# Kernel optimization log

Hardware: AMD Instinct MI355X
Metric: run time of the kernel (lower is better)

The kernel has to match this reference:

```python
import jax, jax.numpy as jnp
import numpy as np

SEQ, B, XD = 2048, 4, 16
D, NH, DFF, L, M = 256, 8, 512, 2, 1024
DH = D // NH
NEG_INF = -1e9  # finite stand-in for -inf (same softmax result, grad-safe)


def setup_inputs() -> dict:
    key = jax.random.key(0)
    ks = iter(jax.random.split(key, 40))

    def w(shape, s=0.02):
        return jax.random.normal(next(ks), shape, dtype=jnp.float32) * s

    return {
        "x": jax.random.normal(next(ks), (SEQ, B, XD), dtype=jnp.float32),
        "y": jax.random.normal(next(ks), (SEQ, B), dtype=jnp.float32),
        "single_eval_pos": M,
        "xenc_w": w((D, XD)), "xenc_b": w((D,)),
        "yenc_w": w((D, 1)), "yenc_b": w((D,)),
        "in_proj_w": w((L, 3 * D, D)), "in_proj_b": w((L, 3 * D)),
        "out_proj_w": w((L, D, D)), "out_proj_b": w((L, D)),
        "ln1_g": jnp.ones((L, D), jnp.float32), "ln1_b": jnp.zeros((L, D), jnp.float32),
        "lin1_w": w((L, DFF, D)), "lin1_b": w((L, DFF)),
        "lin2_w": w((L, D, DFF)), "lin2_b": w((L, D)),
        "ln2_g": jnp.ones((L, D), jnp.float32), "ln2_b": jnp.zeros((L, D), jnp.float32),
        "head_w1": w((DFF, D)), "head_b1": w((DFF,)),
        "head_w2": w((1, DFF)), "head_b2": w((1,)),
    }


def _layer_norm(x, g, b, eps=1e-5):
    mu = jnp.mean(x, axis=-1, keepdims=True)
    var = jnp.var(x, axis=-1, keepdims=True)
    return (x - mu) * jax.lax.rsqrt(var + eps) * g + b


def _forward(x, y, M_, p):
    seq, batch = y.shape
    x_src = x @ p["xenc_w"].T + p["xenc_b"]                     # [seq, b, D]
    y_src = y[..., None] @ p["yenc_w"].T + p["yenc_b"]           # [seq, b, D]
    tokens = jnp.concatenate([x_src[:M_] + y_src[:M_], x_src[M_:]], axis=0)

    # prefix-block + diagonal mask: keep (j < M) or (i == j)
    i = jnp.arange(seq)
    keep = (i[None, :] < M_) | (i[:, None] == i[None, :])
    mask = jnp.where(keep, 0.0, NEG_INF).astype(tokens.dtype)    # [seq, seq]

    h = tokens
    for l in range(p["in_proj_w"].shape[0]):
        qkv = h @ p["in_proj_w"][l].T + p["in_proj_b"][l]        # [seq, b, 3D]
        q, k, v = jnp.split(qkv, 3, axis=-1)
        to_heads = lambda t: t.reshape(seq, batch, NH, DH).transpose(1, 2, 0, 3)
        q, k, v = to_heads(q), to_heads(k), to_heads(v)          # [b, h, s, dh]
        scores = jnp.einsum("bhqd,bhkd->bhqk", q, k) / np.float32(np.sqrt(DH)) + mask
        attn = jax.nn.softmax(scores, axis=-1)
        o = jnp.einsum("bhqk,bhkd->bhqd", attn, v)
        o = o.transpose(2, 0, 1, 3).reshape(seq, batch, D)
        o = o @ p["out_proj_w"][l].T + p["out_proj_b"][l]
        h = _layer_norm(h + o, p["ln1_g"][l], p["ln1_b"][l])      # post-norm
        ff = jax.nn.gelu(h @ p["lin1_w"][l].T + p["lin1_b"][l], approximate=False)
        ff = ff @ p["lin2_w"][l].T + p["lin2_b"][l]
        h = _layer_norm(h + ff, p["ln2_g"][l], p["ln2_b"][l])

    q_out = h[M_:]                                               # [seq-M, b, D]
    hid = jax.nn.gelu(q_out @ p["head_w1"].T + p["head_b1"], approximate=False)
    return hid @ p["head_w2"].T + p["head_b2"]                   # [seq-M, b, 1]


def reference(x, y, single_eval_pos, xenc_w, xenc_b, yenc_w, yenc_b,
              in_proj_w, in_proj_b, out_proj_w, out_proj_b,
              ln1_g, ln1_b, lin1_w, lin1_b, lin2_w, lin2_b, ln2_g, ln2_b,
              head_w1, head_b1, head_w2, head_b2):
    p = dict(xenc_w=xenc_w, xenc_b=xenc_b, yenc_w=yenc_w, yenc_b=yenc_b,
             in_proj_w=in_proj_w, in_proj_b=in_proj_b,
             out_proj_w=out_proj_w, out_proj_b=out_proj_b,
             ln1_g=ln1_g, ln1_b=ln1_b, lin1_w=lin1_w, lin1_b=lin1_b,
             lin2_w=lin2_w, lin2_b=lin2_b, ln2_g=ln2_g, ln2_b=ln2_b,
             head_w1=head_w1, head_b1=head_b1, head_w2=head_w2, head_b2=head_b2)
    return _forward(x, y, int(single_eval_pos), p)
```

## Files before the change

kernel.cpp:

```cpp
#include <hip/hip_runtime.h>
#include <hip/hip_bf16.h>
#include <math.h>

#define SEQ    2048
#define BATCH  4
#define XDIM   16
#define DMODEL 256
#define NHEAD  8
#define DH     32
#define DFF    512
#define NLAYER 2
#define MPOS   1024
#define ROWS   (SEQ*BATCH)

#define ATT_SCALE 0.17677669529663687f
#define BK 32

typedef __attribute__((ext_vector_type(8))) short bf16x8;
typedef __attribute__((ext_vector_type(4))) float f32x4;

__device__ __forceinline__ float gelu_exact(float x) {
    return 0.5f * x * (1.0f + erff(x * 0.70710678118654752f));
}
__device__ __forceinline__ short f2bf(float f) {
    unsigned int u = __float_as_uint(f);
    u += 0x7FFFu + ((u >> 16) & 1u);
    return (short)(u >> 16);
}
__device__ __forceinline__ float bf2f(unsigned short u) {
    return __uint_as_float(((unsigned int)u) << 16);
}
__device__ __forceinline__ void gload16(const unsigned short* g, unsigned short* l) {
    __builtin_amdgcn_global_load_lds(
        (const __attribute__((address_space(1))) unsigned int*)g,
        (__attribute__((address_space(3))) unsigned int*)l, 16, 0, 0);
}
#define VMWAIT(N) asm volatile("s_waitcnt vmcnt(" #N ")" ::: "memory")
__device__ __forceinline__ void pipe_barrier() {
    __builtin_amdgcn_sched_barrier(0);
    __builtin_amdgcn_s_barrier();
    __builtin_amdgcn_sched_barrier(0);
}

__global__ __launch_bounds__(256) void encode_cast(
    const float* __restrict__ x, const float* __restrict__ y,
    const float* __restrict__ xw, const float* __restrict__ xb,
    const float* __restrict__ yw, const float* __restrict__ yb,
    float* __restrict__ h, unsigned short* __restrict__ hb,
    const float* __restrict__ s0, const float* __restrict__ s1,
    const float* __restrict__ s2, const float* __restrict__ s3,
    const float* __restrict__ s4,
    unsigned short* __restrict__ d0, unsigned short* __restrict__ d1,
    unsigned short* __restrict__ d2, unsigned short* __restrict__ d3,
    unsigned short* __restrict__ d4)
{
    if (blockIdx.x < ROWS/4) {
        int g = blockIdx.x;
        int d = threadIdx.x;
        __shared__ float xs[4][XDIM];
        __shared__ float ys[4];
        if (d < 64) xs[d>>4][d&15] = x[(size_t)(g*4 + (d>>4))*XDIM + (d&15)];
        if (d < 4)  ys[d] = y[g*4 + d];
        __syncthreads();
        float wreg[XDIM];
        #pragma unroll
        for (int k = 0; k < XDIM; ++k) wreg[k] = xw[d*XDIM + k];
        const float xbv = xb[d], ywv = yw[d], ybv = yb[d];
        const bool train = (g < MPOS);
        #pragma unroll
        for (int r = 0; r < 4; ++r) {
            int row = g*4 + r;
            float acc = xbv;
            #pragma unroll
            for (int k = 0; k < XDIM; ++k) acc = fmaf(xs[r][k], wreg[k], acc);
            if (train) acc += ys[r]*ywv + ybv;
            h[(size_t)row*DMODEL + d]  = acc;
            hb[(size_t)row*DMODEL + d] = (unsigned short)f2bf(acc);
        }
        return;
    }
    int i = (blockIdx.x - ROWS/4)*256 + threadIdx.x;
    if (i >= 147456) return;
    const float* s; unsigned short* d; int off;
    if      (i <  49152) { s = s0; d = d0; off = i; }
    else if (i <  65536) { s = s1; d = d1; off = i - 49152; }
    else if (i <  98304) { s = s2; d = d2; off = i - 65536; }
    else if (i < 131072) { s = s3; d = d3; off = i - 98304; }
    else                 { s = s4; d = d4; off = i - 131072; }
    float4 a = *(const float4*)(s + (size_t)off*8);
    float4 c = *(const float4*)(s + (size_t)off*8 + 4);
    ushort4 u0, u1;
    u0.x=(unsigned short)f2bf(a.x); u0.y=(unsigned short)f2bf(a.y);
    u0.z=(unsigned short)f2bf(a.z); u0.w=(unsigned short)f2bf(a.w);
    u1.x=(unsigned short)f2bf(c.x); u1.y=(unsigned short)f2bf(c.y);
    u1.z=(unsigned short)f2bf(c.z); u1.w=(unsigned short)f2bf(c.w);
    *(ushort4*)(d + (size_t)off*8)     = u0;
    *(ushort4*)(d + (size_t)off*8 + 4) = u1;
}

__global__ __launch_bounds__(256) void gemm_qkv(
    const unsigned short* __restrict__ A, const unsigned short* __restrict__ B,
    const float* __restrict__ bias,
    unsigned short* __restrict__ Qg, unsigned short* __restrict__ Kg,
    unsigned short* __restrict__ Vg, int K)
{
    __shared__ unsigned short As[3][128][BK];
    __shared__ unsigned short Bs[3][64][BK];
    int tid  = threadIdx.x;
    int w    = tid >> 6, lane = tid & 63;
    int col  = lane & 15, quad = lane >> 4;
    int u    = blockIdx.x >> 3, xcd = blockIdx.x & 7;
    int by   = xcd*8 + u/12, bx = u%12;
    int m0   = by * 128, n0 = bx * 64;
    int l4   = lane >> 2, c8 = (lane & 3) * 8;

    f32x4 acc[2][4];
    #pragma unroll
    for (int i = 0; i < 2; ++i)
        #pragma unroll
        for (int j = 0; j < 4; ++j) acc[i][j] = (f32x4){0.f,0.f,0.f,0.f};

    const unsigned short* ga = A + (size_t)(m0 + w*32 + l4)*K + c8;
    const unsigned short* gb = B + (size_t)(n0 + w*16 + l4)*K + c8;

    const int NS = K / BK;
    gload16(ga,                  &As[0][w*32     ][0]);
    gload16(ga + (size_t)16*K,   &As[0][w*32 + 16][0]);
    gload16(gb,                  &Bs[0][w*16     ][0]);
    gload16(ga + BK,                  &As[1][w*32     ][0]);
    gload16(ga + BK + (size_t)16*K,   &As[1][w*32 + 16][0]);
    gload16(gb + BK,                  &Bs[1][w*16     ][0]);

    int bcur = 0;
    for (int s = 0; s < NS; ++s) {
        if (s == NS - 1) { VMWAIT(0); } else { VMWAIT(3); }
        pipe_barrier();
        if (s + 2 < NS) {
            int bpre = bcur + 2; if (bpre >= 3) bpre -= 3;
            int k2 = (s + 2) * BK;
            gload16(ga + k2,                &As[bpre][w*32     ][0]);
            gload16(ga + k2 + (size_t)16*K, &As[bpre][w*32 + 16][0]);
            gload16(gb + k2,                &Bs[bpre][w*16     ][0]);
        }
        bf16x8 af[2], bfr[4];
        #pragma unroll
        for (int i = 0; i < 2; ++i) af[i]  = *(const bf16x8*)&As[bcur][w*32 + i*16 + col][quad*8];
        #pragma unroll
        for (int j = 0; j < 4; ++j) bfr[j] = *(const bf16x8*)&Bs[bcur][j*16 + col][quad*8];
        #pragma unroll
        for (int i = 0; i < 2; ++i)
            #pragma unroll
            for (int j = 0; j < 4; ++j)
                acc[i][j] = __builtin_amdgcn_mfma_f32_16x16x32_bf16(bfr[j], af[i], acc[i][j], 0, 0, 0);
        bcur = (bcur == 2) ? 0 : bcur + 1;
    }

    int region = n0 >> 8;
    if (region < 2) {
        #pragma unroll
        for (int i = 0; i < 2; ++i) {
            int m = m0 + w*32 + i*16 + col;
            int s = m >> 2, bidx = m & 3;
            #pragma unroll
            for (int j = 0; j < 4; ++j) {
                int ng = n0 + j*16 + quad*4;
                float4 bi = *(const float4*)&bias[ng];
                ushort4 uu;
                uu.x=(unsigned short)f2bf(acc[i][j][0] + bi.x);
                uu.y=(unsigned short)f2bf(acc[i][j][1] + bi.y);
                uu.z=(unsigned short)f2bf(acc[i][j][2] + bi.z);
                uu.w=(unsigned short)f2bf(acc[i][j][3] + bi.w);
                int np = ng - (region << 8);
                int hh = np >> 5, d = np & 31;
                int bh = bidx*NHEAD + hh;
                if (region == 0)
                    *(ushort4*)(Qg + ((size_t)(bh*SEQ + s))*DH + d) = uu;
                else
                    *(ushort4*)(Kg + ((size_t)(bh*SEQ + s))*DH + d) = uu;
            }
        }
    } else {
        __syncthreads();
        unsigned short* T3 = (unsigned short*)As;
        #pragma unroll
        for (int i = 0; i < 2; ++i) {
            int mi = w*32 + i*16 + col;
            int ss = mi >> 2, bidx = mi & 3;
            #pragma unroll
            for (int j = 0; j < 4; ++j) {
                int ni = j*16 + quad*4;
                float4 bi = *(const float4*)&bias[n0 + ni];
                T3[((ni    )*4 + bidx)*32 + ss] = (unsigned short)f2bf(acc[i][j][0] + bi.x);
                T3[((ni + 1)*4 + bidx)*32 + ss] = (unsigned short)f2bf(acc[i][j][1] + bi.y);
                T3[((ni + 2)*4 + bidx)*32 + ss] = (unsigned short)f2bf(acc[i][j][2] + bi.z);
                T3[((ni + 3)*4 + bidx)*32 + ss] = (unsigned short)f2bf(acc[i][j][3] + bi.w);
            }
        }
        __syncthreads();
        int sBase = m0 >> 2;
        #pragma unroll
        for (int r = 0; r < 4; ++r) {
            int chunk = tid + 256*r;
            int l = chunk >> 2, p = chunk & 3;
            int d = l & 31, hh_l = (l >> 5) & 1, bidx = l >> 6;
            int ni = hh_l*32 + d;
            int hh = ((n0 & 255) + ni) >> 5;
            int bh = bidx*NHEAD + hh;
            uint4 val = *(const uint4*)&T3[(ni*4 + bidx)*32 + p*8];
            *(uint4*)(Vg + ((size_t)(bh*DH + d))*SEQ + sBase + p*8) = val;
        }
    }
}

__global__ __launch_bounds__(256) void attn_mfma(
    const unsigned short* __restrict__ Qg,
    const unsigned short* __restrict__ Kg,
    const unsigned short* __restrict__ Vg,
    unsigned short* __restrict__ o)
{
    const int id  = blockIdx.x;
    const int sl  = id >> 3;
    const int bh  = (id & 7) * 4 + (sl >> 4);
    const int qt2 = sl & 15;
    const int h   = bh & 7;
    const int b   = bh >> 3;
    const int q0A = qt2 * 64;
    const int q0B = MPOS + qt2 * 64;
    const int tid  = threadIdx.x;
    const int w    = tid >> 6;
    const int lane = tid & 63;
    const int col  = lane & 15;
    const int quad = lane >> 4;

    __shared__ unsigned short Kt[2][64][40];
    __shared__ unsigned short Vt[2][32][72];
    __shared__ unsigned short PtA[4][16][72];
    __shared__ unsigned short PtB[4][16][72];

    const int qA = q0A + 16*w + col;
    const int qB = q0B + 16*w + col;
    bf16x8 qfA = *(const bf16x8*)(Qg + ((size_t)(bh*SEQ + qA))*DH + quad*8);
    bf16x8 qfB = *(const bf16x8*)(Qg + ((size_t)(bh*SEQ + qB))*DH + quad*8);

    f32x4 O0A = {0.f,0.f,0.f,0.f}, O1A = {0.f,0.f,0.f,0.f};
    f32x4 O0B = {0.f,0.f,0.f,0.f}, O1B = {0.f,0.f,0.f,0.f};
    float lsumA = 0.f, lsumB = 0.f;

    const int kRow = tid >> 2, kCh = (tid & 3) * 8;
    const int vD   = tid >> 3, vCh = (tid & 7) * 8;

    uint4 kreg = *(const uint4*)(Kg + ((size_t)(bh*SEQ + kRow))*DH + kCh);
    uint4 vreg = *(const uint4*)(Vg + ((size_t)(bh*DH + vD))*SEQ + vCh);

    for (int kt = 0; kt < 17; ++kt) {
        const bool self = (kt == 16);
        const int  p    = kt & 1;
        *(uint4*)&Kt[p][kRow][kCh] = kreg;
        *(uint4*)&Vt[p][vD][vCh]   = vreg;
        __syncthreads();
        if (kt < 16) {
            int kn = (kt == 15) ? q0B : (kt + 1)*64;
            kreg = *(const uint4*)(Kg + ((size_t)(bh*SEQ + kn + kRow))*DH + kCh);
            vreg = *(const uint4*)(Vg + ((size_t)(bh*DH + vD))*SEQ + kn + vCh);
        }

        #pragma unroll
        for (int mt = 0; mt < 4; ++mt) {
            bf16x8 kf = *(const bf16x8*)&Kt[p][mt*16 + col][quad*8];
            if (!self) {
                f32x4 stA = {0.f,0.f,0.f,0.f};
                stA = __builtin_amdgcn_mfma_f32_16x16x32_bf16(kf, qfA, stA, 0, 0, 0);
                ushort4 pwA;
                #pragma unroll
                for (int i = 0; i < 4; ++i) {
                    float pv = __expf(stA[i]*ATT_SCALE);
                    unsigned short us = (unsigned short)f2bf(pv);
                    ((unsigned short*)&pwA)[i] = us;
                    lsumA += bf2f(us);
                }
                *(ushort4*)&PtA[w][col][mt*16 + quad*4] = pwA;
            }
            f32x4 stB = {0.f,0.f,0.f,0.f};
            stB = __builtin_amdgcn_mfma_f32_16x16x32_bf16(kf, qfB, stB, 0, 0, 0);
            ushort4 pwB;
            #pragma unroll
            for (int i = 0; i < 4; ++i) {
                float pv = __expf(stB[i]*ATT_SCALE);
                if (self && (mt*16 + quad*4 + i != 16*w + col)) pv = 0.f;
                unsigned short us = (unsigned short)f2bf(pv);
                ((unsigned short*)&pwB)[i] = us;
                lsumB += bf2f(us);
            }
            *(ushort4*)&PtB[w][col][mt*16 + quad*4] = pwB;
        }
        #pragma unroll
        for (int c = 0; c < 2; ++c) {
            bf16x8 v0 = *(const bf16x8*)&Vt[p][col     ][c*32 + quad*8];
            bf16x8 v1 = *(const bf16x8*)&Vt[p][col + 16][c*32 + quad*8];
            if (!self) {
                bf16x8 pfA = *(const bf16x8*)&PtA[w][col][c*32 + quad*8];
                O0A = __builtin_amdgcn_mfma_f32_16x16x32_bf16(v0, pfA, O0A, 0, 0, 0);
                O1A = __builtin_amdgcn_mfma_f32_16x16x32_bf16(v1, pfA, O1A, 0, 0, 0);
            }
            bf16x8 pfB = *(const bf16x8*)&PtB[w][col][c*32 + quad*8];
            O0B = __builtin_amdgcn_mfma_f32_16x16x32_bf16(v0, pfB, O0B, 0, 0, 0);
            O1B = __builtin_amdgcn_mfma_f32_16x16x32_bf16(v1, pfB, O1B, 0, 0, 0);
        }
    }

    lsumA += __shfl_xor(lsumA, 16, 64); lsumA += __shfl_xor(lsumA, 32, 64);
    lsumB += __shfl_xor(lsumB, 16, 64); lsumB += __shfl_xor(lsumB, 32, 64);
    float invA = 1.0f / lsumA, invB = 1.0f / lsumB;
    ushort4 u0, u1;
    #pragma unroll
    for (int i = 0; i < 4; ++i) {
        ((unsigned short*)&u0)[i] = (unsigned short)f2bf(O0A[i]*invA);
        ((unsigned short*)&u1)[i] = (unsigned short)f2bf(O1A[i]*invA);
    }
    unsigned short* opA = o + ((size_t)(qA*BATCH + b))*DMODEL + h*DH;
    *(ushort4*)(opA + quad*4)      = u0;
    *(ushort4*)(opA + 16 + quad*4) = u1;
    #pragma unroll
    for (int i = 0; i < 4; ++i) {
        ((unsigned short*)&u0)[i] = (unsigned short)f2bf(O0B[i]*invB);
        ((unsigned short*)&u1)[i] = (unsigned short)f2bf(O1B[i]*invB);
    }
    unsigned short* opB = o + ((size_t)(qB*BATCH + b))*DMODEL + h*DH;
    *(ushort4*)(opB + quad*4)      = u0;
    *(ushort4*)(opB + 16 + quad*4) = u1;
}

__global__ __launch_bounds__(256) void mlp_fused(
    const unsigned short* __restrict__ attb,
    const unsigned short* __restrict__ Wout, const float* __restrict__ ob,
    const float* __restrict__ g1, const float* __restrict__ be1,
    const unsigned short* __restrict__ W1, const float* __restrict__ fb1,
    const unsigned short* __restrict__ W2, const float* __restrict__ fb2,
    const float* __restrict__ g2, const float* __restrict__ be2,
    float* __restrict__ h, unsigned short* __restrict__ hb,
    const unsigned short* __restrict__ Wh1, const float* __restrict__ hb1,
    const float* __restrict__ hw2, const float* __restrict__ hb2,
    float* __restrict__ out, int doHead)
{
    __shared__ unsigned short Bs[3][256][BK];
    __shared__ unsigned short As[3][2][16][BK];
    __shared__ unsigned short Ht[2][16][264];
    __shared__ unsigned short Pt[2][16][520];
    __shared__ float sP[2][4][16], qP[2][4][16];

    const int tid  = threadIdx.x;
    const int w    = tid >> 6;
    const int lane = tid & 63;
    const int col  = lane & 15;
    const int quad = lane >> 4;
    const int l4   = lane >> 2;
    const int c8   = (lane & 3) * 8;
    const int bid  = blockIdx.x;
    const int m0a  = bid * 16;
    const int m0b  = 4096 + bid * 16;
    const int ma   = m0a + col;
    const int mb   = m0b + col;

    float resid[2][4][4];

    {
        f32x4 acc[2][4];
        #pragma unroll
        for (int g = 0; g < 2; ++g)
            #pragma unroll
            for (int j = 0; j < 4; ++j) acc[g][j] = (f32x4){0.f,0.f,0.f,0.f};

        const unsigned short* ga0 = attb + (size_t)(m0a + l4)*DMODEL + c8;
        const unsigned short* ga1 = attb + (size_t)(m0b + l4)*DMODEL + c8;
        const unsigned short* gb  = Wout + (size_t)(w*64 + l4)*DMODEL + c8;
        const int NS = DMODEL / BK;

        #pragma unroll
        for (int pb = 0; pb < 2; ++pb) {
            int k = pb * BK;
            if (w == 0) {
                gload16(ga0 + k, &As[pb][0][0][0]);
                gload16(ga1 + k, &As[pb][1][0][0]);
            }
            #pragma unroll
            for (int rr = 0; rr < 4; ++rr)
                gload16(gb + k + (size_t)(rr*16)*DMODEL, &Bs[pb][w*64 + rr*16][0]);
        }
        int bcur = 0;
        for (int s = 0; s < NS; ++s) {
            if (s == NS - 1)  { VMWAIT(0); }
            else if (w == 0)  { VMWAIT(6); }
            else              { VMWAIT(4); }
            pipe_barrier();
            if (s + 2 < NS) {
                int bpre = bcur + 2; if (bpre >= 3) bpre -= 3;
                int k2 = (s + 2) * BK;
                if (w == 0) {
                    gload16(ga0 + k2, &As[bpre][0][0][0]);
                    gload16(ga1 + k2, &As[bpre][1][0][0]);
                }
                #pragma unroll
                for (int rr = 0; rr < 4; ++rr)
                    gload16(gb + k2 + (size_t)(rr*16)*DMODEL, &Bs[bpre][w*64 + rr*16][0]);
            }
            bf16x8 af0 = *(const bf16x8*)&As[bcur][0][col][quad*8];
            bf16x8 af1 = *(const bf16x8*)&As[bcur][1][col][quad*8];
            #pragma unroll
            for (int j = 0; j < 4; ++j) {
                bf16x8 bfr = *(const bf16x8*)&Bs[bcur][w*64 + j*16 + col][quad*8];
                acc[0][j] = __builtin_amdgcn_mfma_f32_16x16x32_bf16(bfr, af0, acc[0][j], 0, 0, 0);
                acc[1][j] = __builtin_amdgcn_mfma_f32_16x16x32_bf16(bfr, af1, acc[1][j], 0, 0, 0);
            }
            bcur = (bcur == 2) ? 0 : bcur + 1;
        }

        float ssum[2] = {0.f, 0.f}, qsum[2] = {0.f, 0.f};
        #pragma unroll
        for (int g = 0; g < 2; ++g) {
            int m = g ? mb : ma;
            #pragma unroll
            for (int j = 0; j < 4; ++j) {
                int n = w*64 + j*16 + quad*4;
                float4 bi = *(const float4*)&ob[n];
                float4 hv = *(const float4*)&h[(size_t)m*DMODEL + n];
                #pragma unroll
                for (int i = 0; i < 4; ++i) {
                    float val = acc[g][j][i] + ((const float*)&bi)[i] + ((const float*)&hv)[i];
                    resid[g][j][i] = val;
                    ssum[g] += val; qsum[g] += val*val;
                }
            }
        }
        #pragma unroll
        for (int g = 0; g < 2; ++g) {
            ssum[g] += __shfl_xor(ssum[g], 16, 64); ssum[g] += __shfl_xor(ssum[g], 32, 64);
            qsum[g] += __shfl_xor(qsum[g], 16, 64); qsum[g] += __shfl_xor(qsum[g], 32, 64);
        }
        if (quad == 0) {
            sP[0][w][col] = ssum[0]; qP[0][w][col] = qsum[0];
            sP[1][w][col] = ssum[1]; qP[1][w][col] = qsum[1];
        }
        __syncthreads();
        #pragma unroll
        for (int g = 0; g < 2; ++g) {
            float st = sP[g][0][col] + sP[g][1][col] + sP[g][2][col] + sP[g][3][col];
            float qt = qP[g][0][col] + qP[g][1][col] + qP[g][2][col] + qP[g][3][col];
            float mu   = st * (1.0f/DMODEL);
            float var  = qt * (1.0f/DMODEL) - mu*mu;
            float rstd = rsqrtf(var + 1e-5f);
            #pragma unroll
            for (int j = 0; j < 4; ++j) {
                int n = w*64 + j*16 + quad*4;
                float4 gv = *(const float4*)&g1[n];
                float4 bv = *(const float4*)&be1[n];
                ushort4 u;
                #pragma unroll
                for (int i = 0; i < 4; ++i) {
                    float o = (resid[g][j][i]-mu)*rstd*((const float*)&gv)[i] + ((const float*)&bv)[i];
                    resid[g][j][i] = o;
                    ((unsigned short*)&u)[i] = (unsigned short)f2bf(o);
                }
                *(ushort4*)&Ht[g][col][n] = u;
            }
        }
        __syncthreads();
    }

    #pragma unroll 1
    for (int nh = 0; nh < 2; ++nh) {
        f32x4 acc[2][4];
        #pragma unroll
        for (int g = 0; g < 2; ++g)
            #pragma unroll
            for (int j = 0; j < 4; ++j) acc[g][j] = (f32x4){0.f,0.f,0.f,0.f};
        const unsigned short* gb = W1 + (size_t)(nh*256 + w*64 + l4)*DMODEL + c8;
        const int NS = DMODEL / BK;

        #pragma unroll
        for (int pb = 0; pb < 2; ++pb)
            #pragma unroll
            for (int rr = 0; rr < 4; ++rr)
                gload16(gb + pb*BK + (size_t)(rr*16)*DMODEL, &Bs[pb][w*64 + rr*16][0]);

        int bcur = 0;
        for (int s = 0; s < NS; ++s) {
            if (s == NS - 1) { VMWAIT(0); } else { VMWAIT(4); }
            pipe_barrier();
            if (s + 2 < NS) {
                int bpre = bcur + 2; if (bpre >= 3) bpre -= 3;
                int k2 = (s + 2) * BK;
                #pragma unroll
                for (int rr = 0; rr < 4; ++rr)
                    gload16(gb + k2 + (size_t)(rr*16)*DMODEL, &Bs[bpre][w*64 + rr*16][0]);
            }
            bf16x8 af0 = *(const bf16x8*)&Ht[0][col][s*BK + quad*8];
            bf16x8 af1 = *(const bf16x8*)&Ht[1][col][s*BK + quad*8];
            #pragma unroll
            for (int j = 0; j < 4; ++j) {
                bf16x8 bfr = *(const bf16x8*)&Bs[bcur][w*64 + j*16 + col][quad*8];
                acc[0][j] = __builtin_amdgcn_mfma_f32_16x16x32_bf16(bfr, af0, acc[0][j], 0, 0, 0);
                acc[1][j] = __builtin_amdgcn_mfma_f32_16x16x32_bf16(bfr, af1, acc[1][j], 0, 0, 0);
            }
            bcur = (bcur == 2) ? 0 : bcur + 1;
        }
        #pragma unroll
        for (int g = 0; g < 2; ++g)
            #pragma unroll
            for (int j = 0; j < 4; ++j) {
                int n2 = nh*256 + w*64 + j*16 + quad*4;
                float4 bi = *(const float4*)&fb1[n2];
                ushort4 u;
                #pragma unroll
                for (int i = 0; i < 4; ++i)
                    ((unsigned short*)&u)[i] = (unsigned short)f2bf(gelu_exact(acc[g][j][i] + ((const float*)&bi)[i]));
                *(ushort4*)&Pt[g][col][n2] = u;
            }
        pipe_barrier();
    }

    {
        __syncthreads();
        f32x4 acc[2][4];
        #pragma unroll
        for (int g = 0; g < 2; ++g)
            #pragma unroll
            for (int j = 0; j < 4; ++j) acc[g][j] = (f32x4){0.f,0.f,0.f,0.f};
        const unsigned short* gb = W2 + (size_t)(w*64 + l4)*DFF + c8;
        const int NS = DFF / BK;

        #pragma unroll
        for (int pb = 0; pb < 2; ++pb)
            #pragma unroll
            for (int rr = 0; rr < 4; ++rr)
                gload16(gb + pb*BK + (size_t)(rr*16)*DFF, &Bs[pb][w*64 + rr*16][0]);

        int bcur = 0;
        for (int s = 0; s < NS; ++s) {
            if (s == NS - 1) { VMWAIT(0); } else { VMWAIT(4); }
            pipe_barrier();
            if (s + 2 < NS) {
                int bpre = bcur + 2; if (bpre >= 3) bpre -= 3;
                int k2 = (s + 2) * BK;
                #pragma unroll
                for (int rr = 0; rr < 4; ++rr)
                    gload16(gb + k2 + (size_t)(rr*16)*DFF, &Bs[bpre][w*64 + rr*16][0]);
            }
            bf16x8 af0 = *(const bf16x8*)&Pt[0][col][s*BK + quad*8];
            bf16x8 af1 = *(const bf16x8*)&Pt[1][col][s*BK + quad*8];
            #pragma unroll
            for (int j = 0; j < 4; ++j) {
                bf16x8 bfr = *(const bf16x8*)&Bs[bcur][w*64 + j*16 + col][quad*8];
                acc[0][j] = __builtin_amdgcn_mfma_f32_16x16x32_bf16(bfr, af0, acc[0][j], 0, 0, 0);
                acc[1][j] = __builtin_amdgcn_mfma_f32_16x16x32_bf16(bfr, af1, acc[1][j], 0, 0, 0);
            }
            bcur = (bcur == 2) ? 0 : bcur + 1;
        }

        float ssum[2] = {0.f, 0.f}, qsum[2] = {0.f, 0.f};
        #pragma unroll
        for (int g = 0; g < 2; ++g)
            #pragma unroll
            for (int j = 0; j < 4; ++j) {
                int n = w*64 + j*16 + quad*4;
                float4 bi = *(const float4*)&fb2[n];
                #pragma unroll
                for (int i = 0; i < 4; ++i) {
                    float val = acc[g][j][i] + ((const float*)&bi)[i] + resid[g][j][i];
                    resid[g][j][i] = val;
                    ssum[g] += val; qsum[g] += val*val;
                }
            }
        #pragma unroll
        for (int g = 0; g < 2; ++g) {
            ssum[g] += __shfl_xor(ssum[g], 16, 64); ssum[g] += __shfl_xor(ssum[g], 32, 64);
            qsum[g] += __shfl_xor(qsum[g], 16, 64); qsum[g] += __shfl_xor(qsum[g], 32, 64);
        }
        if (quad == 0) {
            sP[0][w][col] = ssum[0]; qP[0][w][col] = qsum[0];
            sP[1][w][col] = ssum[1]; qP[1][w][col] = qsum[1];
        }
        __syncthreads();
        #pragma unroll
        for (int g = 0; g < 2; ++g) {
            int m = g ? mb : ma;
            float st = sP[g][0][col] + sP[g][1][col] + sP[g][2][col] + sP[g][3][col];
            float qt = qP[g][0][col] + qP[g][1][col] + qP[g][2][col] + qP[g][3][col];
            float mu   = st * (1.0f/DMODEL);
            float var  = qt * (1.0f/DMODEL) - mu*mu;
            float rstd = rsqrtf(var + 1e-5f);
            #pragma unroll
            for (int j = 0; j < 4; ++j) {
                int n = w*64 + j*16 + quad*4;
                float4 gv = *(const float4*)&g2[n];
                float4 bv = *(const float4*)&be2[n];
                float4 o;
                ushort4 u;
                #pragma unroll
                for (int i = 0; i < 4; ++i) {
                    float ov = (resid[g][j][i]-mu)*rstd*((const float*)&gv)[i] + ((const float*)&bv)[i];
                    ((float*)&o)[i] = ov;
                    ((unsigned short*)&u)[i] = (unsigned short)f2bf(ov);
                }
                *(float4*)&h[(size_t)m*DMODEL + n] = o;
                *(ushort4*)(hb + (size_t)m*DMODEL + n) = u;
                *(ushort4*)&Ht[g][col][n] = u;
            }
        }
        __syncthreads();
    }

    if (doHead) {
        float sdot = 0.f;
        #pragma unroll 1
        for (int nh = 0; nh < 2; ++nh) {
            f32x4 acc[4];
            #pragma unroll
            for (int j = 0; j < 4; ++j) acc[j] = (f32x4){0.f,0.f,0.f,0.f};
            const unsigned short* gb = Wh1 + (size_t)(nh*256 + w*64 + l4)*DMODEL + c8;
            const int NS = DMODEL / BK;

            #pragma unroll
            for (int pb = 0; pb < 2; ++pb)
                #pragma unroll
                for (int rr = 0; rr < 4; ++rr)
                    gload16(gb + pb*BK + (size_t)(rr*16)*DMODEL, &Bs[pb][w*64 + rr*16][0]);

            int bcur = 0;
            for (int s = 0; s < NS; ++s) {
                if (s == NS - 1) { VMWAIT(0); } else { VMWAIT(4); }
                pipe_barrier();
                if (s + 2 < NS) {
                    int bpre = bcur + 2; if (bpre >= 3) bpre -= 3;
                    int k2 = (s + 2) * BK;
                    #pragma unroll
                    for (int rr = 0; rr < 4; ++rr)
                        gload16(gb + k2 + (size_t)(rr*16)*DMODEL, &Bs[bpre][w*64 + rr*16][0]);
                }
                bf16x8 af = *(const bf16x8*)&Ht[1][col][s*BK + quad*8];
                #pragma unroll
                for (int j = 0; j < 4; ++j) {
                    bf16x8 bfr = *(const bf16x8*)&Bs[bcur][w*64 + j*16 + col][quad*8];
                    acc[j] = __builtin_amdgcn_mfma_f32_16x16x32_bf16(bfr, af, acc[j], 0, 0, 0);
                }
                bcur = (bcur == 2) ? 0 : bcur + 1;
            }
            #pragma unroll
            for (int j = 0; j < 4; ++j) {
                int n2 = nh*256 + w*64 + j*16 + quad*4;
                float4 b1v = *(const float4*)&hb1[n2];
                float4 w2v = *(const float4*)&hw2[n2];
                #pragma unroll
                for (int i = 0; i < 4; ++i)
                    sdot += gelu_exact(acc[j][i] + ((const float*)&b1v)[i]) * ((const float*)&w2v)[i];
            }
            pipe_barrier();
        }
        sdot += __shfl_xor(sdot, 16, 64); sdot += __shfl_xor(sdot, 32, 64);
        if (quad == 0) sP[0][w][col] = sdot;
        __syncthreads();
        if (tid < 16)
            out[bid*16 + tid] = sP[0][0][tid] + sP[0][1][tid] + sP[0][2][tid] + sP[0][3][tid] + hb2[0];
    }
}

extern "C" void kernel_launch(void* const* d_in, const int* in_sizes, int n_in,
                              void* d_out, int out_size, void* d_ws, size_t ws_size,
                              hipStream_t stream)
{
    const float* x        = (const float*)d_in[0];
    const float* y        = (const float*)d_in[1];
    const float* xenc_w   = (const float*)d_in[3];
    const float* xenc_b   = (const float*)d_in[4];
    const float* yenc_w   = (const float*)d_in[5];
    const float* yenc_b   = (const float*)d_in[6];
    const float* in_proj_w  = (const float*)d_in[7];
    const float* in_proj_b  = (const float*)d_in[8];
    const float* out_proj_w = (const float*)d_in[9];
    const float* out_proj_b = (const float*)d_in[10];
    const float* ln1_g    = (const float*)d_in[11];
    const float* ln1_b    = (const float*)d_in[12];
    const float* lin1_w   = (const float*)d_in[13];
    const float* lin1_b   = (const float*)d_in[14];
    const float* lin2_w   = (const float*)d_in[15];
    const float* lin2_b   = (const float*)d_in[16];
    const float* ln2_g    = (const float*)d_in[17];
    const float* ln2_b    = (const float*)d_in[18];
    const float* head_w1  = (const float*)d_in[19];
    const float* head_b1  = (const float*)d_in[20];
    const float* head_w2  = (const float*)d_in[21];
    const float* head_b2  = (const float*)d_in[22];
    float* out = (float*)d_out;

    float* ws  = (float*)d_ws;
    float* h    = ws;
    unsigned short* hb    = (unsigned short*)(h + (size_t)ROWS*DMODEL);
    unsigned short* attb  = hb    + (size_t)ROWS*DMODEL;
    unsigned short* Qg    = attb  + (size_t)ROWS*DMODEL;
    unsigned short* Kg    = Qg    + (size_t)BATCH*NHEAD*SEQ*DH;
    unsigned short* Vg    = Kg    + (size_t)BATCH*NHEAD*SEQ*DH;
    unsigned short* Wqkv  = Vg    + (size_t)BATCH*NHEAD*SEQ*DH;
    unsigned short* Wout  = Wqkv  + (size_t)NLAYER*3*DMODEL*DMODEL;
    unsigned short* Wl1   = Wout  + (size_t)NLAYER*DMODEL*DMODEL;
    unsigned short* Wl2   = Wl1   + (size_t)NLAYER*DFF*DMODEL;
    unsigned short* Wh1   = Wl2   + (size_t)NLAYER*DMODEL*DFF;

    encode_cast<<<ROWS/4 + 576, 256, 0, stream>>>(
        x, y, xenc_w, xenc_b, yenc_w, yenc_b, h, hb,
        in_proj_w, out_proj_w, lin1_w, lin2_w, head_w1,
        Wqkv, Wout, Wl1, Wl2, Wh1);

    for (int l = 0; l < NLAYER; ++l) {
        gemm_qkv<<<768, 256, 0, stream>>>(
            hb, Wqkv + (size_t)l*3*DMODEL*DMODEL, in_proj_b + l*3*DMODEL,
            Qg, Kg, Vg, DMODEL);
        attn_mfma<<<512, 256, 0, stream>>>(Qg, Kg, Vg, attb);
        mlp_fused<<<256, 256, 0, stream>>>(
            attb,
            Wout + (size_t)l*DMODEL*DMODEL, out_proj_b + l*DMODEL,
            ln1_g + l*DMODEL, ln1_b + l*DMODEL,
            Wl1 + (size_t)l*DFF*DMODEL, lin1_b + l*DFF,
            Wl2 + (size_t)l*DMODEL*DFF, lin2_b + l*DMODEL,
            ln2_g + l*DMODEL, ln2_b + l*DMODEL,
            h, hb,
            Wh1, head_b1, head_w2, head_b2,
            out, (l == NLAYER-1) ? 1 : 0);
    }
}
```

Before: 258.9 us.

## Fuse layer-1 QKV projection into layer-0 MLP kernel epilogue

For the first layer, the fused MLP kernel now also computes the next layer's QKV projection. It reuses the normalized hidden tile still held in shared memory (Ht) and writes Q, K and V directly in head layout, which removes one gemm_qkv launch and its reread of hb. The cost is more work per block on only 256 blocks instead of 768. The V writes are scalar transposed stores, which may be poorly coalesced.

```diff
diff --git a/kernel.cpp b/kernel.cpp
--- a/kernel.cpp
+++ b/kernel.cpp
@@ -340,7 +340,10 @@
     float* __restrict__ h, unsigned short* __restrict__ hb,
     const unsigned short* __restrict__ Wh1, const float* __restrict__ hb1,
     const float* __restrict__ hw2, const float* __restrict__ hb2,
-    float* __restrict__ out, int doHead)
+    float* __restrict__ out, int doHead,
+    const unsigned short* __restrict__ Wq, const float* __restrict__ qbias,
+    unsigned short* __restrict__ Qg, unsigned short* __restrict__ Kg,
+    unsigned short* __restrict__ Vg, int doQkv)
 {
     __shared__ unsigned short Bs[3][256][BK];
     __shared__ unsigned short As[3][2][16][BK];
@@ -660,6 +663,76 @@
         __syncthreads();
         if (tid < 16)
             out[bid*16 + tid] = sP[0][0][tid] + sP[0][1][tid] + sP[0][2][tid] + sP[0][3][tid] + hb2[0];
+    }
+
+    if (doQkv) {
+        #pragma unroll 1
+        for (int r = 0; r < 3; ++r) {
+            f32x4 acc[2][4];
+            #pragma unroll
+            for (int g = 0; g < 2; ++g)
+                #pragma unroll
+                for (int j = 0; j < 4; ++j) acc[g][j] = (f32x4){0.f,0.f,0.f,0.f};
+            const unsigned short* gb = Wq + (size_t)(r*256 + w*64 + l4)*DMODEL + c8;
+            const int NS = DMODEL / BK;
+
+            #pragma unroll
+            for (int pb = 0; pb < 2; ++pb)
+                #pragma unroll
+                for (int rr = 0; rr < 4; ++rr)
+                    gload16(gb + pb*BK + (size_t)(rr*16)*DMODEL, &Bs[pb][w*64 + rr*16][0]);
+
+            int bcur = 0;
+            for (int s = 0; s < NS; ++s) {
+                if (s == NS - 1) { VMWAIT(0); } else { VMWAIT(4); }
+                pipe_barrier();
+                if (s + 2 < NS) {
+                    int bpre = bcur + 2; if (bpre >= 3) bpre -= 3;
+                    int k2 = (s + 2) * BK;
+                    #pragma unroll
+                    for (int rr = 0; rr < 4; ++rr)
+                        gload16(gb + k2 + (size_t)(rr*16)*DMODEL, &Bs[bpre][w*64 + rr*16][0]);
+                }
+                bf16x8 af0 = *(const bf16x8*)&Ht[0][col][s*BK + quad*8];
+                bf16x8 af1 = *(const bf16x8*)&Ht[1][col][s*BK + quad*8];
+                #pragma unroll
+                for (int j = 0; j < 4; ++j) {
+                    bf16x8 bfr = *(const bf16x8*)&Bs[bcur][w*64 + j*16 + col][quad*8];
+                    acc[0][j] = __builtin_amdgcn_mfma_f32_16x16x32_bf16(bfr, af0, acc[0][j], 0, 0, 0);
+                    acc[1][j] = __builtin_amdgcn_mfma_f32_16x16x32_bf16(bfr, af1, acc[1][j], 0, 0, 0);
+                }
+                bcur = (bcur == 2) ? 0 : bcur + 1;
+            }
+
+            #pragma unroll
+            for (int g = 0; g < 2; ++g) {
+                int m = (g ? m0b : m0a) + col;
+                int ss = m >> 2, bidx = m & 3;
+                #pragma unroll
+                for (int j = 0; j < 4; ++j) {
+                    int n32 = w*64 + j*16 + quad*4;
+                    float4 bi = *(const float4*)&qbias[r*256 + n32];
+                    ushort4 u;
+                    u.x = (unsigned short)f2bf(acc[g][j][0] + bi.x);
+                    u.y = (unsigned short)f2bf(acc[g][j][1] + bi.y);
+                    u.z = (unsigned short)f2bf(acc[g][j][2] + bi.z);
+                    u.w = (unsigned short)f2bf(acc[g][j][3] + bi.w);
+                    int hh = n32 >> 5, d = n32 & 31;
+                    int bh = bidx*NHEAD + hh;
+                    if (r == 0)
+                        *(ushort4*)(Qg + ((size_t)(bh*SEQ + ss))*DH + d) = u;
+                    else if (r == 1)
+                        *(ushort4*)(Kg + ((size_t)(bh*SEQ + ss))*DH + d) = u;
+                    else {
+                        Vg[((size_t)(bh*DH + d    ))*SEQ + ss] = u.x;
+                        Vg[((size_t)(bh*DH + d + 1))*SEQ + ss] = u.y;
+                        Vg[((size_t)(bh*DH + d + 2))*SEQ + ss] = u.z;
+                        Vg[((size_t)(bh*DH + d + 3))*SEQ + ss] = u.w;
+                    }
+                }
+            }
+            pipe_barrier();
+        }
     }
 }
 
@@ -710,9 +783,9 @@
         Wqkv, Wout, Wl1, Wl2, Wh1);
 
     for (int l = 0; l < NLAYER; ++l) {
-        gemm_qkv<<<768, 256, 0, stream>>>(
-            hb, Wqkv + (size_t)l*3*DMODEL*DMODEL, in_proj_b + l*3*DMODEL,
-            Qg, Kg, Vg, DMODEL);
+        if (l == 0)
+            gemm_qkv<<<768, 256, 0, stream>>>(
+                hb, Wqkv, in_proj_b, Qg, Kg, Vg, DMODEL);
         attn_mfma<<<512, 256, 0, stream>>>(Qg, Kg, Vg, attb);
         mlp_fused<<<256, 256, 0, stream>>>(
             attb,
@@ -723,6 +796,8 @@
             ln2_g + l*DMODEL, ln2_b + l*DMODEL,
             h, hb,
             Wh1, head_b1, head_w2, head_b2,
-            out, (l == NLAYER-1) ? 1 : 0);
-    }
-}
+            out, (l == NLAYER-1) ? 1 : 0,
+            Wqkv + (size_t)3*DMODEL*DMODEL, in_proj_b + 3*DMODEL,
+            Qg, Kg, Vg, (l == 0) ? 1 : 0);
+    }
+}
```

New measurement: 265.8 us. +2.7%, slower.

## Widen mlp_fused K-tile to 64 with XOR-swizzled LDS and aliased A/P buffers

Applied to the files above, without the earlier changes.

Doubles the K step of every GEMM stage in the fused MLP kernel from 32 to 64, which halves the number of pipeline barriers and waits per GEMM. Weight and activation tiles are stored in LDS with an XOR swizzle on 16-byte chunks so that MFMA fragment reads avoid bank conflicts. All four waves now share the activation-tile loads, where before only wave 0 issued them. The As staging buffer and the Pt GELU buffer share one aliased LDS region to offset the larger Bs. The cost is more LDS per block and more loads in flight per stage, which could reduce occupancy.

```diff
diff --git a/kernel.cpp b/kernel.cpp
--- a/kernel.cpp
+++ b/kernel.cpp
@@ -342,19 +342,23 @@
     const float* __restrict__ hw2, const float* __restrict__ hb2,
     float* __restrict__ out, int doHead)
 {
-    __shared__ unsigned short Bs[3][256][BK];
-    __shared__ unsigned short As[3][2][16][BK];
+    __shared__ unsigned short Bs[3][256][64];
+    __shared__ __align__(16) unsigned char smem_u[33280];
     __shared__ unsigned short Ht[2][16][264];
-    __shared__ unsigned short Pt[2][16][520];
     __shared__ float sP[2][4][16], qP[2][4][16];
+
+    typedef unsigned short AsT[2][16][64];
+    AsT* As = reinterpret_cast<AsT*>(smem_u);
+    typedef unsigned short PtT[16][520];
+    PtT* Pt = reinterpret_cast<PtT*>(smem_u);
 
     const int tid  = threadIdx.x;
     const int w    = tid >> 6;
     const int lane = tid & 63;
     const int col  = lane & 15;
     const int quad = lane >> 4;
-    const int l4   = lane >> 2;
-    const int c8   = (lane & 3) * 8;
+    const int l8   = lane >> 3;
+    const int c8s  = (((lane & 7) ^ l8) * 8);
     const int bid  = blockIdx.x;
     const int m0a  = bid * 16;
     const int m0b  = 4096 + bid * 16;
@@ -370,46 +374,42 @@
             #pragma unroll
             for (int j = 0; j < 4; ++j) acc[g][j] = (f32x4){0.f,0.f,0.f,0.f};
 
-        const unsigned short* ga0 = attb + (size_t)(m0a + l4)*DMODEL + c8;
-        const unsigned short* ga1 = attb + (size_t)(m0b + l4)*DMODEL + c8;
-        const unsigned short* gb  = Wout + (size_t)(w*64 + l4)*DMODEL + c8;
-        const int NS = DMODEL / BK;
+        const int gr = w >> 1;
+        const unsigned short* gaw = attb + (size_t)((gr ? m0b : m0a) + (w&1)*8 + l8)*DMODEL + c8s;
+        const unsigned short* gb  = Wout + (size_t)(w*64 + l8)*DMODEL + c8s;
+        const int NS = DMODEL / 64;
 
         #pragma unroll
         for (int pb = 0; pb < 2; ++pb) {
-            int k = pb * BK;
-            if (w == 0) {
-                gload16(ga0 + k, &As[pb][0][0][0]);
-                gload16(ga1 + k, &As[pb][1][0][0]);
-            }
-            #pragma unroll
-            for (int rr = 0; rr < 4; ++rr)
-                gload16(gb + k + (size_t)(rr*16)*DMODEL, &Bs[pb][w*64 + rr*16][0]);
+            int k = pb * 64;
+            gload16(gaw + k, &As[pb][gr][(w&1)*8][0]);
+            #pragma unroll
+            for (int t = 0; t < 8; ++t)
+                gload16(gb + k + (size_t)(t*8)*DMODEL, &Bs[pb][w*64 + t*8][0]);
         }
         int bcur = 0;
         for (int s = 0; s < NS; ++s) {
-            if (s == NS - 1)  { VMWAIT(0); }
-            else if (w == 0)  { VMWAIT(6); }
-            else              { VMWAIT(4); }
+            if (s == NS - 1) { VMWAIT(0); } else { VMWAIT(9); }
             pipe_barrier();
             if (s + 2 < NS) {
                 int bpre = bcur + 2; if (bpre >= 3) bpre -= 3;
-                int k2 = (s + 2) * BK;
-                if (w == 0) {
-                    gload16(ga0 + k2, &As[bpre][0][0][0]);
-                    gload16(ga1 + k2, &As[bpre][1][0][0]);
-                }
-                #pragma unroll
-                for (int rr = 0; rr < 4; ++rr)
-                    gload16(gb + k2 + (size_t)(rr*16)*DMODEL, &Bs[bpre][w*64 + rr*16][0]);
-            }
-            bf16x8 af0 = *(const bf16x8*)&As[bcur][0][col][quad*8];
-            bf16x8 af1 = *(const bf16x8*)&As[bcur][1][col][quad*8];
-            #pragma unroll
-            for (int j = 0; j < 4; ++j) {
-                bf16x8 bfr = *(const bf16x8*)&Bs[bcur][w*64 + j*16 + col][quad*8];
-                acc[0][j] = __builtin_amdgcn_mfma_f32_16x16x32_bf16(bfr, af0, acc[0][j], 0, 0, 0);
-                acc[1][j] = __builtin_amdgcn_mfma_f32_16x16x32_bf16(bfr, af1, acc[1][j], 0, 0, 0);
+                int k2 = (s + 2) * 64;
+                gload16(gaw + k2, &As[bpre][gr][(w&1)*8][0]);
+                #pragma unroll
+                for (int t = 0; t < 8; ++t)
+                    gload16(gb + k2 + (size_t)(t*8)*DMODEL, &Bs[bpre][w*64 + t*8][0]);
+            }
+            #pragma unroll
+            for (int kk = 0; kk < 2; ++kk) {
+                const int so = (((kk*4 + quad) ^ (col & 7)) * 8);
+                bf16x8 af0 = *(const bf16x8*)&As[bcur][0][col][so];
+                bf16x8 af1 = *(const bf16x8*)&As[bcur][1][col][so];
+                #pragma unroll
+                for (int j = 0; j < 4; ++j) {
+                    bf16x8 bfr = *(const bf16x8*)&Bs[bcur][w*64 + j*16 + col][so];
+                    acc[0][j] = __builtin_amdgcn_mfma_f32_16x16x32_bf16(bfr, af0, acc[0][j], 0, 0, 0);
+                    acc[1][j] = __builtin_amdgcn_mfma_f32_16x16x32_bf16(bfr, af1, acc[1][j], 0, 0, 0);
+                }
             }
             bcur = (bcur == 2) ? 0 : bcur + 1;
         }
@@ -473,33 +473,37 @@
         for (int g = 0; g < 2; ++g)
             #pragma unroll
             for (int j = 0; j < 4; ++j) acc[g][j] = (f32x4){0.f,0.f,0.f,0.f};
-        const unsigned short* gb = W1 + (size_t)(nh*256 + w*64 + l4)*DMODEL + c8;
-        const int NS = DMODEL / BK;
+        const unsigned short* gb = W1 + (size_t)(nh*256 + w*64 + l8)*DMODEL + c8s;
+        const int NS = DMODEL / 64;
 
         #pragma unroll
         for (int pb = 0; pb < 2; ++pb)
             #pragma unroll
-            for (int rr = 0; rr < 4; ++rr)
-                gload16(gb + pb*BK + (size_t)(rr*16)*DMODEL, &Bs[pb][w*64 + rr*16][0]);
+            for (int t = 0; t < 8; ++t)
+                gload16(gb + pb*64 + (size_t)(t*8)*DMODEL, &Bs[pb][w*64 + t*8][0]);
 
         int bcur = 0;
         for (int s = 0; s < NS; ++s) {
-            if (s == NS - 1) { VMWAIT(0); } else { VMWAIT(4); }
+            if (s == NS - 1) { VMWAIT(0); } else { VMWAIT(8); }
             pipe_barrier();
             if (s + 2 < NS) {
                 int bpre = bcur + 2; if (bpre >= 3) bpre -= 3;
-                int k2 = (s + 2) * BK;
-                #pragma unroll
-                for (int rr = 0; rr < 4; ++rr)
-                    gload16(gb + k2 + (size_t)(rr*16)*DMODEL, &Bs[bpre][w*64 + rr*16][0]);
-            }
-            bf16x8 af0 = *(const bf16x8*)&Ht[0][col][s*BK + quad*8];
-            bf16x8 af1 = *(const bf16x8*)&Ht[1][col][s*BK + quad*8];
-            #pragma unroll
-            for (int j = 0; j < 4; ++j) {
-                bf16x8 bfr = *(const bf16x8*)&Bs[bcur][w*64 + j*16 + col][quad*8];
-                acc[0][j] = __builtin_amdgcn_mfma_f32_16x16x32_bf16(bfr, af0, acc[0][j], 0, 0, 0);
-                acc[1][j] = __builtin_amdgcn_mfma_f32_16x16x32_bf16(bfr, af1, acc[1][j], 0, 0, 0);
+                int k2 = (s + 2) * 64;
+                #pragma unroll
+                for (int t = 0; t < 8; ++t)
+                    gload16(gb + k2 + (size_t)(t*8)*DMODEL, &Bs[bpre][w*64 + t*8][0]);
+            }
+            #pragma unroll
+            for (int kk = 0; kk < 2; ++kk) {
+                const int so = (((kk*4 + quad) ^ (col & 7)) * 8);
+                bf16x8 af0 = *(const bf16x8*)&Ht[0][col][s*64 + kk*32 + quad*8];
+                bf16x8 af1 = *(const bf16x8*)&Ht[1][col][s*64 + kk*32 + quad*8];
+                #pragma unroll
+                for (int j = 0; j < 4; ++j) {
+                    bf16x8 bfr = *(const bf16x8*)&Bs[bcur][w*64 + j*16 + col][so];
+                    acc[0][j] = __builtin_amdgcn_mfma_f32_16x16x32_bf16(bfr, af0, acc[0][j], 0, 0, 0);
+                    acc[1][j] = __builtin_amdgcn_mfma_f32_16x16x32_bf16(bfr, af1, acc[1][j], 0, 0, 0);
+                }
             }
             bcur = (bcur == 2) ? 0 : bcur + 1;
         }
@@ -525,33 +529,37 @@
         for (int g = 0; g < 2; ++g)
             #pragma unroll
             for (int j = 0; j < 4; ++j) acc[g][j] = (f32x4){0.f,0.f,0.f,0.f};
-        const unsigned short* gb = W2 + (size_t)(w*64 + l4)*DFF + c8;
-        const int NS = DFF / BK;
+        const unsigned short* gb = W2 + (size_t)(w*64 + l8)*DFF + c8s;
+        const int NS = DFF / 64;
 
         #pragma unroll
         for (int pb = 0; pb < 2; ++pb)
             #pragma unroll
-            for (int rr = 0; rr < 4; ++rr)
-                gload16(gb + pb*BK + (size_t)(rr*16)*DFF, &Bs[pb][w*64 + rr*16][0]);
+            for (int t = 0; t < 8; ++t)
+                gload16(gb + pb*64 + (size_t)(t*8)*DFF, &Bs[pb][w*64 + t*8][0]);
 
         int bcur = 0;
         for (int s = 0; s < NS; ++s) {
-            if (s == NS - 1) { VMWAIT(0); } else { VMWAIT(4); }
+            if (s == NS - 1) { VMWAIT(0); } else { VMWAIT(8); }
             pipe_barrier();
             if (s + 2 < NS) {
                 int bpre = bcur + 2; if (bpre >= 3) bpre -= 3;
-                int k2 = (s + 2) * BK;
-                #pragma unroll
-                for (int rr = 0; rr < 4; ++rr)
-                    gload16(gb + k2 + (size_t)(rr*16)*DFF, &Bs[bpre][w*64 + rr*16][0]);
-            }
-            bf16x8 af0 = *(const bf16x8*)&Pt[0][col][s*BK + quad*8];
-            bf16x8 af1 = *(const bf16x8*)&Pt[1][col][s*BK + quad*8];
-            #pragma unroll
-            for (int j = 0; j < 4; ++j) {
-                bf16x8 bfr = *(const bf16x8*)&Bs[bcur][w*64 + j*16 + col][quad*8];
-                acc[0][j] = __builtin_amdgcn_mfma_f32_16x16x32_bf16(bfr, af0, acc[0][j], 0, 0, 0);
-                acc[1][j] = __builtin_amdgcn_mfma_f32_16x16x32_bf16(bfr, af1, acc[1][j], 0, 0, 0);
+                int k2 = (s + 2) * 64;
+                #pragma unroll
+                for (int t = 0; t < 8; ++t)
+                    gload16(gb + k2 + (size_t)(t*8)*DFF, &Bs[bpre][w*64 + t*8][0]);
+            }
+            #pragma unroll
+            for (int kk = 0; kk < 2; ++kk) {
+                const int so = (((kk*4 + quad) ^ (col & 7)) * 8);
+                bf16x8 af0 = *(const bf16x8*)&Pt[0][col][s*64 + kk*32 + quad*8];
+                bf16x8 af1 = *(const bf16x8*)&Pt[1][col][s*64 + kk*32 + quad*8];
+                #pragma unroll
+                for (int j = 0; j < 4; ++j) {
+                    bf16x8 bfr = *(const bf16x8*)&Bs[bcur][w*64 + j*16 + col][so];
+                    acc[0][j] = __builtin_amdgcn_mfma_f32_16x16x32_bf16(bfr, af0, acc[0][j], 0, 0, 0);
+                    acc[1][j] = __builtin_amdgcn_mfma_f32_16x16x32_bf16(bfr, af1, acc[1][j], 0, 0, 0);
+                }
             }
             bcur = (bcur == 2) ? 0 : bcur + 1;
         }
@@ -616,31 +624,35 @@
             f32x4 acc[4];
             #pragma unroll
             for (int j = 0; j < 4; ++j) acc[j] = (f32x4){0.f,0.f,0.f,0.f};
-            const unsigned short* gb = Wh1 + (size_t)(nh*256 + w*64 + l4)*DMODEL + c8;
-            const int NS = DMODEL / BK;
+            const unsigned short* gb = Wh1 + (size_t)(nh*256 + w*64 + l8)*DMODEL + c8s;
+            const int NS = DMODEL / 64;
 
             #pragma unroll
             for (int pb = 0; pb < 2; ++pb)
                 #pragma unroll
-                for (int rr = 0; rr < 4; ++rr)
-                    gload16(gb + pb*BK + (size_t)(rr*16)*DMODEL, &Bs[pb][w*64 + rr*16][0]);
+                for (int t = 0; t < 8; ++t)
+                    gload16(gb + pb*64 + (size_t)(t*8)*DMODEL, &Bs[pb][w*64 + t*8][0]);
 
             int bcur = 0;
             for (int s = 0; s < NS; ++s) {
-                if (s == NS - 1) { VMWAIT(0); } else { VMWAIT(4); }
+                if (s == NS - 1) { VMWAIT(0); } else { VMWAIT(8); }
                 pipe_barrier();
                 if (s + 2 < NS) {
                     int bpre = bcur + 2; if (bpre >= 3) bpre -= 3;
-                    int k2 = (s + 2) * BK;
+                    int k2 = (s + 2) * 64;
                     #pragma unroll
-                    for (int rr = 0; rr < 4; ++rr)
-                        gload16(gb + k2 + (size_t)(rr*16)*DMODEL, &Bs[bpre][w*64 + rr*16][0]);
-                }
-                bf16x8 af = *(const bf16x8*)&Ht[1][col][s*BK + quad*8];
-                #pragma unroll
-                for (int j = 0; j < 4; ++j) {
-                    bf16x8 bfr = *(const bf16x8*)&Bs[bcur][w*64 + j*16 + col][quad*8];
-                    acc[j] = __builtin_amdgcn_mfma_f32_16x16x32_bf16(bfr, af, acc[j], 0, 0, 0);
+                    for (int t = 0; t < 8; ++t)
+                        gload16(gb + k2 + (size_t)(t*8)*DMODEL, &Bs[bpre][w*64 + t*8][0]);
+                }
+                #pragma unroll
+                for (int kk = 0; kk < 2; ++kk) {
+                    const int so = (((kk*4 + quad) ^ (col & 7)) * 8);
+                    bf16x8 af = *(const bf16x8*)&Ht[1][col][s*64 + kk*32 + quad*8];
+                    #pragma unroll
+                    for (int j = 0; j < 4; ++j) {
+                        bf16x8 bfr = *(const bf16x8*)&Bs[bcur][w*64 + j*16 + col][so];
+                        acc[j] = __builtin_amdgcn_mfma_f32_16x16x32_bf16(bfr, af, acc[j], 0, 0, 0);
+                    }
                 }
                 bcur = (bcur == 2) ? 0 : bcur + 1;
             }
```

After: 249.4 us. 3.7% less time.
